# Performance work log

Measured on AMD Instinct MI355X. Metric: run time of the kernel, lower is better.

Reference implementation:

```python
import jax, jax.numpy as jnp
import numpy as np

EMBED_DIM = 512
NUM_HEADS = 8
HEAD_DIM = EMBED_DIM // NUM_HEADS
FFN_DIM = 4 * EMBED_DIM
B, S = 4, 2048
LN_EPS = 1e-5


def _linear_params(key, fan_in, fan_out):
    kw, kb = jax.random.split(key)
    bound = 1.0 / np.sqrt(fan_in)
    W = jax.random.uniform(kw, (fan_in, fan_out), jnp.float32, -bound, bound)
    b = jax.random.uniform(kb, (fan_out,), jnp.float32, -bound, bound)
    return W, b


def setup_inputs() -> dict:
    key = jax.random.key(0)
    ks = jax.random.split(key, 10)
    query = jax.random.normal(ks[0], (B, S, EMBED_DIM), jnp.float32)
    key_t = jax.random.normal(ks[1], (B, S, EMBED_DIM), jnp.float32)
    value = jax.random.normal(ks[2], (B, S, EMBED_DIM), jnp.float32)
    Wq, bq = _linear_params(ks[3], EMBED_DIM, EMBED_DIM)
    Wk, bk = _linear_params(ks[4], EMBED_DIM, EMBED_DIM)
    Wv, bv = _linear_params(ks[5], EMBED_DIM, EMBED_DIM)
    Wo, bo = _linear_params(ks[6], EMBED_DIM, EMBED_DIM)
    W1, b1 = _linear_params(ks[7], EMBED_DIM, FFN_DIM)
    W2, b2 = _linear_params(ks[8], FFN_DIM, EMBED_DIM)
    g1 = jnp.ones((EMBED_DIM,), jnp.float32); be1 = jnp.zeros((EMBED_DIM,), jnp.float32)
    g2 = jnp.ones((EMBED_DIM,), jnp.float32); be2 = jnp.zeros((EMBED_DIM,), jnp.float32)
    return dict(query=query, key=key_t, value=value,
                Wq=Wq, bq=bq, Wk=Wk, bk=bk, Wv=Wv, bv=bv, Wo=Wo, bo=bo,
                g1=g1, be1=be1, g2=g2, be2=be2,
                W1=W1, b1=b1, W2=W2, b2=b2)


def _layernorm(x, g, b):
    mu = jnp.mean(x, axis=-1, keepdims=True)
    var = jnp.mean(jnp.square(x - mu), axis=-1, keepdims=True)
    return (x - mu) * jax.lax.rsqrt(var + LN_EPS) * g + b


def reference(query, key, value, Wq, bq, Wk, bk, Wv, bv, Wo, bo,
              g1, be1, g2, be2, W1, b1, W2, b2):
    b_, s_ = query.shape[:2]
    # projections -> [B, H, S, Dh]
    Q = (query @ Wq + bq).reshape(b_, -1, NUM_HEADS, HEAD_DIM).transpose(0, 2, 1, 3)
    K = (key @ Wk + bk).reshape(b_, -1, NUM_HEADS, HEAD_DIM).transpose(0, 2, 1, 3)
    V = (value @ Wv + bv).reshape(b_, -1, NUM_HEADS, HEAD_DIM).transpose(0, 2, 1, 3)
    scores = jnp.einsum('bhqd,bhkd->bhqk', Q, K) / jnp.sqrt(jnp.float32(HEAD_DIM))
    attn = jax.nn.softmax(scores, axis=-1)  # dropout is eval-mode identity
    ctx = jnp.einsum('bhqk,bhkd->bhqd', attn, V)
    ctx = ctx.transpose(0, 2, 1, 3).reshape(b_, -1, EMBED_DIM)
    out = ctx @ Wo + bo
    out = _layernorm(query + out, g1, be1)
    ffn = jax.nn.gelu(out @ W1 + b1, approximate=False) @ W2 + b2
    return _layernorm(out + ffn, g2, be2)
```

## Files before the change

### kernel.cpp

```cpp
#include <hip/hip_runtime.h>
#include <hip/hip_bf16.h>
#include <math.h>

#define EMBED 512
#define NHEAD 8
#define HDIM 64
#define FFN 2048
#define BB 4
#define SS 2048
#define MROWS (BB*SS)
#define NB ((size_t)MROWS * EMBED)
#define LN_EPS 1e-5f
#define QSCALE 0.180336880111f

typedef __attribute__((ext_vector_type(8))) short short8;
typedef __attribute__((ext_vector_type(4))) float floatx4;

__device__ inline float bf2f(__hip_bfloat16 x) { return __bfloat162float(x); }
__device__ inline __hip_bfloat16 f2bf(float x) { return __float2bfloat16(x); }

__device__ inline float gelu_f(float x) {
    return 0.5f * x * (1.0f + erff(x * 0.70710678118654752f));
}

__device__ inline void async_copy16(const void* g, void* l) {
    __builtin_amdgcn_global_load_lds(
        (const __attribute__((address_space(1))) void*)g,
        (__attribute__((address_space(3))) void*)l, 16, 0, 0);
}

__device__ inline int sane_f(float v) {
    return (v == v) && (fabsf(v) > 0x1p-40f) && (fabsf(v) < 0x1p40f);
}

__global__ void detect_kernel(const void* __restrict__ q, int* __restrict__ flag) {
    const float* qf = (const float*)q;
    int lane = threadIdx.x;
    float v = qf[lane * 1024 + 7];
    bool ok = sane_f(v);
    unsigned long long m = __ballot(ok);
    if (lane == 0) *flag = (__popcll(m) >= 32) ? 1 : 0;
}

__global__ __launch_bounds__(256) void prep_kernel(
    const void* __restrict__ query, const void* __restrict__ keyi, const void* __restrict__ vali,
    const void* __restrict__ Wq, const void* __restrict__ Wk, const void* __restrict__ Wv,
    const void* __restrict__ Wo, const void* __restrict__ W1, const void* __restrict__ W2,
    const void* __restrict__ bq, const void* __restrict__ bk, const void* __restrict__ bv,
    const void* __restrict__ bo, const void* __restrict__ b1, const void* __restrict__ b2,
    const void* __restrict__ g1, const void* __restrict__ be1,
    const void* __restrict__ g2, const void* __restrict__ be2,
    __hip_bfloat16* __restrict__ qkvbf,
    __hip_bfloat16* __restrict__ Wcat,
    __hip_bfloat16* __restrict__ biasb)
{
    __shared__ __hip_bfloat16 L[64][65];
    const int f32 = sane_f(((const float*)query)[7]) + sane_f(((const float*)query)[1031]) +
                    sane_f(((const float*)query)[200003]) + sane_f(((const float*)query)[1000003]) >= 3;
    const int t = threadIdx.x;
    const int blk = blockIdx.x;

    if (blk < 6144) {
        size_t pos = ((size_t)blk * 256 + t) * 8;
        int sel = (int)(pos >> 22);
        size_t off = pos & (NB - 1);
        const void* src = sel == 0 ? query : sel == 1 ? keyi : vali;
        if (f32) {
            const float* s = (const float*)src + off;
            float4 f0 = *reinterpret_cast<const float4*>(s);
            float4 f1 = *reinterpret_cast<const float4*>(s + 4);
            alignas(16) __hip_bfloat16 h[8] = {
                f2bf(f0.x), f2bf(f0.y), f2bf(f0.z), f2bf(f0.w),
                f2bf(f1.x), f2bf(f1.y), f2bf(f1.z), f2bf(f1.w)};
            *reinterpret_cast<uint4*>(qkvbf + pos) = *reinterpret_cast<const uint4*>(h);
        } else {
            *reinterpret_cast<uint4*>(qkvbf + pos) =
                *reinterpret_cast<const uint4*>((const __hip_bfloat16*)src + off);
        }
        return;
    }

    const void* src; __hip_bfloat16* dst; int R, C, r0, c0;
    if (blk < 6400) {
        int b2i = blk - 6144; src = W1; dst = Wcat + 4 * 512 * 512;
        R = 512; C = 2048; r0 = (b2i >> 5) * 64; c0 = (b2i & 31) * 64;
    } else if (blk < 6656) {
        int b3 = blk - 6400; src = W2; dst = Wcat + 4 * 512 * 512 + 512 * 2048;
        R = 2048; C = 512; r0 = (b3 >> 3) * 64; c0 = (b3 & 7) * 64;
    } else if (blk < 6912) {
        int b4 = blk - 6656; int which = b4 >> 6; int tile = b4 & 63;
        src = which == 0 ? Wq : which == 1 ? Wk : which == 2 ? Wv : Wo;
        dst = Wcat + (size_t)which * 512 * 512;
        R = 512; C = 512; r0 = (tile >> 3) * 64; c0 = (tile & 7) * 64;
    } else {
        const void* srcs[10] = {bq, bk, bv, bo, b1, b2, g1, be1, g2, be2};
        const int offs[10] = {0, 512, 1024, 1536, 2048, 4096, 4608, 5120, 5632, 6144};
        const int lens[10] = {512, 512, 512, 512, 2048, 512, 512, 512, 512, 512};
        for (int a = 0; a < 10; ++a)
            for (int i = t; i < lens[a]; i += 256)
                biasb[offs[a] + i] = f32 ? f2bf(((const float*)srcs[a])[i])
                                         : ((const __hip_bfloat16*)srcs[a])[i];
        return;
    }
    for (int c = t; c < 4096; c += 256) {
        int lr = c >> 6, lc = c & 63;
        L[lr][lc] = f32 ? f2bf(((const float*)src)[(size_t)(r0 + lr) * C + c0 + lc])
                        : ((const __hip_bfloat16*)src)[(size_t)(r0 + lr) * C + c0 + lc];
    }
    __syncthreads();
    for (int c = t; c < 4096; c += 256) {
        int lr = c >> 6, lc = c & 63;
        dst[(size_t)(c0 + lr) * R + r0 + lc] = L[lc][lr];
    }
}

template<int ACT, int BIAS>
__global__ __launch_bounds__(256) void gemm_bt_lds_kernel(
    const __hip_bfloat16* __restrict__ A,
    const __hip_bfloat16* __restrict__ Bt,
    const __hip_bfloat16* __restrict__ bias,
    __hip_bfloat16* __restrict__ C,
    int M, int N, int K, int ksplit)
{
    const int bm = blockIdx.x * 128;
    const int bn = blockIdx.y * 128;
    int kbeg = 0, kend = K;
    if (BIAS == 0) {
        kbeg = blockIdx.z * ksplit;
        kend = kbeg + ksplit;
        C += (size_t)blockIdx.z * NB;
    }
    const int t = threadIdx.x;
    const int wave = t >> 6, lane = t & 63;
    const int wm = (wave >> 1) * 64, wn = (wave & 1) * 64;
    const int quad = lane >> 4, r = lane & 15;

    __shared__ alignas(16) __hip_bfloat16 As[2][128 * 32];
    __shared__ alignas(16) __hip_bfloat16 Bs[2][128 * 32];

    floatx4 acc[4][4];
    #pragma unroll
    for (int i = 0; i < 4; ++i)
        #pragma unroll
        for (int j = 0; j < 4; ++j)
            acc[i][j] = (floatx4){0.f, 0.f, 0.f, 0.f};

    const int c0 = wave * 128;

    for (int kt = kbeg; kt < kend; kt += 64) {
        #pragma unroll
        for (int h = 0; h < 2; ++h) {
            #pragma unroll
            for (int it = 0; it < 2; ++it) {
                int c = c0 + it * 64 + lane;
                int row = c >> 2, col = (c & 3) * 8;
                async_copy16(A + (size_t)(bm + row) * K + kt + h * 32 + col,
                             As[h] + (size_t)(c0 + it * 64) * 8);
                async_copy16(Bt + (size_t)(bn + row) * K + kt + h * 32 + col,
                             Bs[h] + (size_t)(c0 + it * 64) * 8);
            }
        }
        __syncthreads();
        #pragma unroll
        for (int h = 0; h < 2; ++h) {
            short8 af[4], bfr[4];
            #pragma unroll
            for (int i = 0; i < 4; ++i)
                af[i] = *reinterpret_cast<const short8*>(&As[h][(wm + i * 16 + r) * 32 + quad * 8]);
            #pragma unroll
            for (int j = 0; j < 4; ++j)
                bfr[j] = *reinterpret_cast<const short8*>(&Bs[h][(wn + j * 16 + r) * 32 + quad * 8]);
            #pragma unroll
            for (int i = 0; i < 4; ++i)
                #pragma unroll
                for (int j = 0; j < 4; ++j)
                    acc[i][j] = __builtin_amdgcn_mfma_f32_16x16x32_bf16(af[i], bfr[j], acc[i][j], 0, 0, 0);
        }
        __syncthreads();
    }

    #pragma unroll
    for (int j = 0; j < 4; ++j) {
        const int n = bn + wn + j * 16 + r;
        float bvv = BIAS ? bf2f(bias[n]) : 0.f;
        #pragma unroll
        for (int i = 0; i < 4; ++i) {
            #pragma unroll
            for (int v = 0; v < 4; ++v) {
                int m = bm + wm + i * 16 + quad * 4 + v;
                float x = acc[i][j][v] + bvv;
                if (ACT == 1) x = gelu_f(x);
                C[(size_t)m * N + n] = f2bf(x);
            }
        }
    }
}

__global__ __launch_bounds__(256) void gemm_qkv_fused_kernel(
    const __hip_bfloat16* __restrict__ Acat,
    const __hip_bfloat16* __restrict__ Wcat,
    const __hip_bfloat16* __restrict__ biascat,
    __hip_bfloat16* __restrict__ Ocat)
{
    const int sel = blockIdx.x >> 6;
    const __hip_bfloat16* A = Acat + (size_t)sel * NB;
    const __hip_bfloat16* Bt = Wcat + (size_t)sel * 512 * 512;
    const __hip_bfloat16* bias = biascat + sel * 512;
    __hip_bfloat16* C = Ocat + (size_t)sel * NB;

    const int bm = (blockIdx.x & 63) * 128;
    const int bn = blockIdx.y * 128;
    const int t = threadIdx.x;
    const int wave = t >> 6, lane = t & 63;
    const int wm = (wave >> 1) * 64, wn = (wave & 1) * 64;
    const int quad = lane >> 4, r = lane & 15;
    const int K = EMBED, N = EMBED;

    __shared__ alignas(16) __hip_bfloat16 As[2][128 * 32];
    __shared__ alignas(16) __hip_bfloat16 Bs[2][128 * 32];

    floatx4 acc[4][4];
    #pragma unroll
    for (int i = 0; i < 4; ++i)
        #pragma unroll
        for (int j = 0; j < 4; ++j)
            acc[i][j] = (floatx4){0.f, 0.f, 0.f, 0.f};

    const int c0 = wave * 128;

    for (int kt = 0; kt < K; kt += 64) {
        #pragma unroll
        for (int h = 0; h < 2; ++h) {
            #pragma unroll
            for (int it = 0; it < 2; ++it) {
                int c = c0 + it * 64 + lane;
                int row = c >> 2, col = (c & 3) * 8;
                async_copy16(A + (size_t)(bm + row) * K + kt + h * 32 + col,
                             As[h] + (size_t)(c0 + it * 64) * 8);
                async_copy16(Bt + (size_t)(bn + row) * K + kt + h * 32 + col,
                             Bs[h] + (size_t)(c0 + it * 64) * 8);
            }
        }
        __syncthreads();
        #pragma unroll
        for (int h = 0; h < 2; ++h) {
            short8 af[4], bfr[4];
            #pragma unroll
            for (int i = 0; i < 4; ++i)
                af[i] = *reinterpret_cast<const short8*>(&As[h][(wm + i * 16 + r) * 32 + quad * 8]);
            #pragma unroll
            for (int j = 0; j < 4; ++j)
                bfr[j] = *reinterpret_cast<const short8*>(&Bs[h][(wn + j * 16 + r) * 32 + quad * 8]);
            #pragma unroll
            for (int i = 0; i < 4; ++i)
                #pragma unroll
                for (int j = 0; j < 4; ++j)
                    acc[i][j] = __builtin_amdgcn_mfma_f32_16x16x32_bf16(af[i], bfr[j], acc[i][j], 0, 0, 0);
        }
        __syncthreads();
    }

    #pragma unroll
    for (int j = 0; j < 4; ++j) {
        const int n = bn + wn + j * 16 + r;
        const float bvv = bf2f(bias[n]);
        #pragma unroll
        for (int i = 0; i < 4; ++i) {
            #pragma unroll
            for (int v = 0; v < 4; ++v) {
                int m = bm + wm + i * 16 + quad * 4 + v;
                C[(size_t)m * N + n] = f2bf(acc[i][j][v] + bvv);
            }
        }
    }
}

__global__ __launch_bounds__(256) void vtrans_kernel(
    const __hip_bfloat16* __restrict__ Vb, __hip_bfloat16* __restrict__ Vt)
{
    const int bh = blockIdx.y;
    const int b = bh >> 3, h = bh & 7;
    const int s0 = blockIdx.x * 64;
    __shared__ alignas(16) __hip_bfloat16 L[64][72];
    const int t = threadIdx.x;
    for (int c = t; c < 512; c += 256) {
        int row = c >> 3, g = c & 7;
        *reinterpret_cast<uint4*>(&L[row][g * 8]) =
            *reinterpret_cast<const uint4*>(Vb + (size_t)(b * SS + s0 + row) * EMBED + h * 64 + g * 8);
    }
    __syncthreads();
    for (int c = t; c < 512; c += 256) {
        int d = c >> 3, g = c & 7;
        alignas(16) __hip_bfloat16 tmp[8];
        #pragma unroll
        for (int j = 0; j < 8; ++j) tmp[j] = L[g * 8 + j][d];
        *reinterpret_cast<uint4*>(Vt + ((size_t)bh * 64 + d) * SS + s0 + g * 8) =
            *reinterpret_cast<const uint4*>(tmp);
    }
}

__global__ __launch_bounds__(256) void attn_mfma_kernel(
    const __hip_bfloat16* __restrict__ Qg,
    const __hip_bfloat16* __restrict__ Kg,
    const __hip_bfloat16* __restrict__ Vt,
    __hip_bfloat16* __restrict__ Apart0,
    __hip_bfloat16* __restrict__ Apart1,
    float* __restrict__ lbuf)
{
    const int bh = blockIdx.y;
    const int b = bh >> 3, h = bh & 7;
    const int q0 = blockIdx.x * 128;
    const int z = blockIdx.z;
    const int t = threadIdx.x;
    const int w = t >> 6, lane = t & 63;
    const int quad = lane >> 4, r = lane & 15;

    __shared__ alignas(16) __hip_bfloat16 Ks[2][64 * 32];
    __shared__ alignas(16) __hip_bfloat16 Vs[2][64 * 32];
    __shared__ alignas(16) __hip_bfloat16 Ps[4][32][72];

    const size_t bbase = (size_t)b * SS * EMBED;
    const size_t hoff = (size_t)h * HDIM;
    const size_t vtbase = (size_t)bh * HDIM * SS;

    short8 aq[2][2];
    #pragma unroll
    for (int s = 0; s < 2; ++s) {
        const __hip_bfloat16* qrow = Qg + bbase + (size_t)(q0 + w * 32 + s * 16 + r) * EMBED + hoff;
        short8 t0 = *reinterpret_cast<const short8*>(qrow + quad * 8);
        short8 t1 = *reinterpret_cast<const short8*>(qrow + 32 + quad * 8);
        #pragma unroll
        for (int i = 0; i < 8; ++i) {
            ((__hip_bfloat16*)&aq[s][0])[i] = f2bf(bf2f(((const __hip_bfloat16*)&t0)[i]) * QSCALE);
            ((__hip_bfloat16*)&aq[s][1])[i] = f2bf(bf2f(((const __hip_bfloat16*)&t1)[i]) * QSCALE);
        }
    }

    const short one = 0x3F80;
    const short8 bones = {one, one, one, one, one, one, one, one};

    const int tensor = w >> 1, slab = w & 1;
    const int srow = lane >> 2, scol = (lane & 3) * 8;

    floatx4 o0[4], o1[4], l0a, l1a;
    #pragma unroll
    for (int nt = 0; nt < 4; ++nt) {
        o0[nt] = (floatx4){0.f, 0.f, 0.f, 0.f};
        o1[nt] = (floatx4){0.f, 0.f, 0.f, 0.f};
    }
    l0a = (floatx4){0.f, 0.f, 0.f, 0.f};
    l1a = (floatx4){0.f, 0.f, 0.f, 0.f};

    const int kbeg = z * (SS / 2), kend = kbeg + SS / 2;
    const __hip_bfloat16* kp[4];
    const __hip_bfloat16* vp[4];
    #pragma unroll
    for (int g = 0; g < 4; ++g) {
        int row = g * 16 + srow;
        kp[g] = Kg + bbase + (size_t)(kbeg + row) * EMBED + hoff + slab * 32 + scol;
        vp[g] = Vt + vtbase + (size_t)row * SS + kbeg + slab * 32 + scol;
    }

    for (int kt = kbeg; kt < kend; kt += 64) {
        __syncthreads();
        if (tensor == 0) {
            #pragma unroll
            for (int g = 0; g < 4; ++g) {
                async_copy16(kp[g], &Ks[slab][g * 512]);
                kp[g] += 64 * EMBED;
            }
        } else {
            #pragma unroll
            for (int g = 0; g < 4; ++g) {
                async_copy16(vp[g], &Vs[slab][g * 512]);
                vp[g] += 64;
            }
        }
        __syncthreads();

        floatx4 s0[4], s1[4];
        #pragma unroll
        for (int nt = 0; nt < 4; ++nt) {
            s0[nt] = (floatx4){0.f, 0.f, 0.f, 0.f};
            s1[nt] = (floatx4){0.f, 0.f, 0.f, 0.f};
        }
        #pragma unroll
        for (int nt = 0; nt < 4; ++nt) {
            short8 ak0 = *reinterpret_cast<const short8*>(&Ks[0][(nt * 16 + r) * 32 + quad * 8]);
            short8 ak1 = *reinterpret_cast<const short8*>(&Ks[1][(nt * 16 + r) * 32 + quad * 8]);
            s0[nt] = __builtin_amdgcn_mfma_f32_16x16x32_bf16(ak0, aq[0][0], s0[nt], 0, 0, 0);
            s0[nt] = __builtin_amdgcn_mfma_f32_16x16x32_bf16(ak1, aq[0][1], s0[nt], 0, 0, 0);
            s1[nt] = __builtin_amdgcn_mfma_f32_16x16x32_bf16(ak0, aq[1][0], s1[nt], 0, 0, 0);
            s1[nt] = __builtin_amdgcn_mfma_f32_16x16x32_bf16(ak1, aq[1][1], s1[nt], 0, 0, 0);
        }

        #pragma unroll
        for (int s = 0; s < 2; ++s) {
            floatx4* sc = s == 0 ? s0 : s1;
            #pragma unroll
            for (int nt = 0; nt < 4; ++nt) {
                float p0 = exp2f(sc[nt][0]), p1 = exp2f(sc[nt][1]);
                float p2 = exp2f(sc[nt][2]), p3 = exp2f(sc[nt][3]);
                __hip_bfloat162 pa = __float22bfloat162_rn(make_float2(p0, p1));
                __hip_bfloat162 pb = __float22bfloat162_rn(make_float2(p2, p3));
                uint2 u;
                u.x = *reinterpret_cast<unsigned*>(&pa);
                u.y = *reinterpret_cast<unsigned*>(&pb);
                *reinterpret_cast<uint2*>(&Ps[w][s * 16 + r][nt * 16 + quad * 4]) = u;
            }
        }

        short8 ap00 = *reinterpret_cast<const short8*>(&Ps[w][r][quad * 8]);
        short8 ap01 = *reinterpret_cast<const short8*>(&Ps[w][r][32 + quad * 8]);
        short8 ap10 = *reinterpret_cast<const short8*>(&Ps[w][16 + r][quad * 8]);
        short8 ap11 = *reinterpret_cast<const short8*>(&Ps[w][16 + r][32 + quad * 8]);
        #pragma unroll
        for (int nt = 0; nt < 4; ++nt) {
            short8 bv0 = *reinterpret_cast<const short8*>(&Vs[0][(nt * 16 + r) * 32 + quad * 8]);
            short8 bv1 = *reinterpret_cast<const short8*>(&Vs[1][(nt * 16 + r) * 32 + quad * 8]);
            o0[nt] = __builtin_amdgcn_mfma_f32_16x16x32_bf16(ap00, bv0, o0[nt], 0, 0, 0);
            o0[nt] = __builtin_amdgcn_mfma_f32_16x16x32_bf16(ap01, bv1, o0[nt], 0, 0, 0);
            o1[nt] = __builtin_amdgcn_mfma_f32_16x16x32_bf16(ap10, bv0, o1[nt], 0, 0, 0);
            o1[nt] = __builtin_amdgcn_mfma_f32_16x16x32_bf16(ap11, bv1, o1[nt], 0, 0, 0);
        }
        l0a = __builtin_amdgcn_mfma_f32_16x16x32_bf16(ap00, bones, l0a, 0, 0, 0);
        l0a = __builtin_amdgcn_mfma_f32_16x16x32_bf16(ap01, bones, l0a, 0, 0, 0);
        l1a = __builtin_amdgcn_mfma_f32_16x16x32_bf16(ap10, bones, l1a, 0, 0, 0);
        l1a = __builtin_amdgcn_mfma_f32_16x16x32_bf16(ap11, bones, l1a, 0, 0, 0);
    }

    __hip_bfloat16* Ap = z == 0 ? Apart0 : Apart1;
    #pragma unroll
    for (int s = 0; s < 2; ++s) {
        floatx4* oa = s == 0 ? o0 : o1;
        floatx4 la = s == 0 ? l0a : l1a;
        #pragma unroll
        for (int v = 0; v < 4; ++v) {
            int q = q0 + w * 32 + s * 16 + quad * 4 + v;
            __hip_bfloat16* orow = Ap + bbase + (size_t)q * EMBED + hoff;
            #pragma unroll
            for (int nt = 0; nt < 4; ++nt)
                orow[nt * 16 + r] = f2bf(oa[nt][v]);
            if (r == 0)
                lbuf[((size_t)z * 32 + bh) * SS + q] = la[v];
        }
    }
}

__global__ __launch_bounds__(256) void attn_combine_kernel(
    const __hip_bfloat16* __restrict__ Apart0,
    const __hip_bfloat16* __restrict__ Apart1,
    const float* __restrict__ lbuf,
    __hip_bfloat16* __restrict__ ctx)
{
    const int bh = blockIdx.y;
    const int b = bh >> 3, h = bh & 7;
    const int q0 = blockIdx.x * 64;
    const int t = threadIdx.x;
    __shared__ float winv[64];

    if (t < 64) {
        float l0 = lbuf[(size_t)bh * SS + q0 + t];
        float l1 = lbuf[((size_t)32 + bh) * SS + q0 + t];
        winv[t] = 1.0f / (l0 + l1);
    }
    __syncthreads();

    const size_t base = (size_t)b * SS * EMBED + (size_t)h * HDIM;
    for (int c = t; c < 512; c += 256) {
        int q = c >> 3, d8 = (c & 7) * 8;
        size_t off = base + (size_t)(q0 + q) * EMBED + d8;
        short8 a0v = *reinterpret_cast<const short8*>(Apart0 + off);
        short8 a1v = *reinterpret_cast<const short8*>(Apart1 + off);
        float si = winv[q];
        alignas(16) __hip_bfloat16 o[8];
        #pragma unroll
        for (int j = 0; j < 8; ++j) {
            float x0 = bf2f(((const __hip_bfloat16*)&a0v)[j]);
            float x1 = bf2f(((const __hip_bfloat16*)&a1v)[j]);
            o[j] = f2bf((x0 + x1) * si);
        }
        *reinterpret_cast<uint4*>(ctx + off) = *reinterpret_cast<const uint4*>(o);
    }
}

__device__ inline float block_reduce_sum(float v, float* sbuf) {
    #pragma unroll
    for (int off = 32; off; off >>= 1) v += __shfl_xor(v, off, 64);
    int wave = threadIdx.x >> 6;
    if ((threadIdx.x & 63) == 0) sbuf[wave] = v;
    __syncthreads();
    float r = sbuf[0] + sbuf[1] + sbuf[2] + sbuf[3];
    __syncthreads();
    return r;
}

template<int OUT32>
__global__ __launch_bounds__(256) void add_ln_split_kernel(
    const __hip_bfloat16* __restrict__ X,
    const __hip_bfloat16* __restrict__ Y0,
    const __hip_bfloat16* __restrict__ Y1,
    const __hip_bfloat16* __restrict__ bias,
    const __hip_bfloat16* __restrict__ g,
    const __hip_bfloat16* __restrict__ bt,
    void* __restrict__ out,
    const int* __restrict__ dflag)
{
    __shared__ float sbuf[4];
    const int row = blockIdx.x;
    const size_t base = (size_t)row * EMBED;
    const int t = threadIdx.x;

    float x0 = bf2f(X[base + t]) + bf2f(Y0[base + t]) + bf2f(Y1[base + t]) + bf2f(bias[t]);
    float x1 = bf2f(X[base + t + 256]) + bf2f(Y0[base + t + 256]) + bf2f(Y1[base + t + 256]) + bf2f(bias[t + 256]);
    float s = block_reduce_sum(x0 + x1, sbuf);
    float mu = s * (1.0f / EMBED);
    float d0 = x0 - mu, d1 = x1 - mu;
    float vs = block_reduce_sum(d0 * d0 + d1 * d1, sbuf);
    float rstd = rsqrtf(vs * (1.0f / EMBED) + LN_EPS);

    float o0 = d0 * rstd * bf2f(g[t]) + bf2f(bt[t]);
    float o1 = d1 * rstd * bf2f(g[t + 256]) + bf2f(bt[t + 256]);
    if (OUT32 && *dflag) {
        ((float*)out)[base + t] = o0;
        ((float*)out)[base + t + 256] = o1;
    } else {
        ((__hip_bfloat16*)out)[base + t] = f2bf(o0);
        ((__hip_bfloat16*)out)[base + t + 256] = f2bf(o1);
    }
}

extern "C" void kernel_launch(void* const* d_in, const int* in_sizes, int n_in,
                              void* d_out, int out_size, void* d_ws, size_t ws_size,
                              hipStream_t stream)
{
    (void)in_sizes; (void)n_in; (void)out_size; (void)ws_size;

    const void* query = d_in[0];
    const void* keyi  = d_in[1];
    const void* vali  = d_in[2];
    const void* Wq = d_in[3];  const void* bq = d_in[4];
    const void* Wk = d_in[5];  const void* bk = d_in[6];
    const void* Wv = d_in[7];  const void* bv = d_in[8];
    const void* Wo = d_in[9];  const void* bo = d_in[10];
    const void* g1 = d_in[11]; const void* be1 = d_in[12];
    const void* g2 = d_in[13]; const void* be2 = d_in[14];
    const void* W1 = d_in[15]; const void* b1 = d_in[16];
    const void* W2 = d_in[17]; const void* b2 = d_in[18];

    int* dflag = (int*)d_ws;
    __hip_bfloat16* biasb = (__hip_bfloat16*)((char*)d_ws + 64);
    __hip_bfloat16* Wcat = biasb + 8192;
    __hip_bfloat16* buf = Wcat + 4 * 512 * 512 + 2 * 512 * 2048;
    __hip_bfloat16* bqkvb = biasb;
    __hip_bfloat16* bob  = biasb + 1536;
    __hip_bfloat16* b1b  = biasb + 2048;
    __hip_bfloat16* b2b  = biasb + 4096;
    __hip_bfloat16* g1b  = biasb + 4608;
    __hip_bfloat16* be1b = biasb + 5120;
    __hip_bfloat16* g2b  = biasb + 5632;
    __hip_bfloat16* be2b = biasb + 6144;
    __hip_bfloat16* qkvbf  = buf;
    __hip_bfloat16* QKVo   = buf + 3 * NB;
    __hip_bfloat16* Qb = QKVo;
    __hip_bfloat16* Kb = QKVo + NB;
    __hip_bfloat16* Vb = QKVo + 2 * NB;
    __hip_bfloat16* Vt     = buf + 1 * NB;
    __hip_bfloat16* Apart0 = buf + 2 * NB;
    __hip_bfloat16* Apart1 = buf + 6 * NB;
    float*          lbuf   = (float*)(buf + 7 * NB);
    __hip_bfloat16* ctx    = buf + 3 * NB;
    __hip_bfloat16* Yw     = buf + 4 * NB;
    __hip_bfloat16* x1     = buf + 3 * NB;
    __hip_bfloat16* hbf    = buf + 4 * NB;
    __hip_bfloat16* Yf     = buf + 1 * NB;

    detect_kernel<<<1, 64, 0, stream>>>(query, dflag);

    prep_kernel<<<6913, 256, 0, stream>>>(
        query, keyi, vali, Wq, Wk, Wv, Wo, W1, W2,
        bq, bk, bv, bo, b1, b2, g1, be1, g2, be2,
        qkvbf, Wcat, biasb);

    gemm_qkv_fused_kernel<<<dim3(192, 4), 256, 0, stream>>>(qkvbf, Wcat, bqkvb, QKVo);

    vtrans_kernel<<<dim3(SS / 64, BB * NHEAD), 256, 0, stream>>>(Vb, Vt);

    attn_mfma_kernel<<<dim3(SS / 128, BB * NHEAD, 2), 256, 0, stream>>>(
        Qb, Kb, Vt, Apart0, Apart1, lbuf);
    attn_combine_kernel<<<dim3(SS / 64, BB * NHEAD), 256, 0, stream>>>(
        Apart0, Apart1, lbuf, ctx);

    gemm_bt_lds_kernel<0, 0><<<dim3(MROWS / 128, EMBED / 128, 2), 256, 0, stream>>>(
        ctx, Wcat + 3 * 512 * 512, nullptr, Yw, MROWS, EMBED, EMBED, EMBED / 2);
    add_ln_split_kernel<0><<<MROWS, 256, 0, stream>>>(
        qkvbf, Yw, Yw + NB, bob, g1b, be1b, x1, dflag);

    gemm_bt_lds_kernel<1, 1><<<dim3(MROWS / 128, FFN / 128), 256, 0, stream>>>(
        x1, Wcat + 4 * 512 * 512, b1b, hbf, MROWS, FFN, EMBED, 0);
    gemm_bt_lds_kernel<0, 0><<<dim3(MROWS / 128, EMBED / 128, 2), 256, 0, stream>>>(
        hbf, Wcat + 4 * 512 * 512 + 512 * 2048, nullptr, Yf, MROWS, EMBED, FFN, FFN / 2);
    add_ln_split_kernel<1><<<MROWS, 256, 0, stream>>>(
        x1, Yf, Yf + NB, b2b, g2b, be2b, d_out, dflag);
}
```

Measured before the change: 343.4 us.

## Swizzle attention K/V LDS layout and make layernorm one wave per row

The K and V tiles in LDS are stored with an XOR swizzle on the 16-byte column chunk, and the MFMA operand reads apply the same swizzle, so a wave's reads spread across LDS banks instead of conflicting. The add+layernorm kernel now gives each 64-lane wave one row with 8 elements per lane. It loads with 16-byte vector accesses and reduces with wave shuffles only, so the shared-memory block reductions and barriers go away. Risk: the swizzle must match the async copy store path exactly, or K and V will be read in the wrong order.

After: 331.7 us. -3.4%, faster.

```diff
diff --git a/kernel.cpp b/kernel.cpp
--- a/kernel.cpp
+++ b/kernel.cpp
@@ -340,7 +340,9 @@
     const short8 bones = {one, one, one, one, one, one, one, one};
 
     const int tensor = w >> 1, slab = w & 1;
-    const int srow = lane >> 2, scol = (lane & 3) * 8;
+    const int srow = lane >> 2;
+    const int scol = (((lane & 3) ^ ((srow >> 1) & 3)) * 8);
+    const int cs = ((r >> 1) & 3) * 8;
 
     floatx4 o0[4], o1[4], l0a, l1a;
     #pragma unroll
@@ -386,8 +388,8 @@
         }
         #pragma unroll
         for (int nt = 0; nt < 4; ++nt) {
-            short8 ak0 = *reinterpret_cast<const short8*>(&Ks[0][(nt * 16 + r) * 32 + quad * 8]);
-            short8 ak1 = *reinterpret_cast<const short8*>(&Ks[1][(nt * 16 + r) * 32 + quad * 8]);
+            short8 ak0 = *reinterpret_cast<const short8*>(&Ks[0][(nt * 16 + r) * 32 + (quad * 8 ^ cs)]);
+            short8 ak1 = *reinterpret_cast<const short8*>(&Ks[1][(nt * 16 + r) * 32 + (quad * 8 ^ cs)]);
             s0[nt] = __builtin_amdgcn_mfma_f32_16x16x32_bf16(ak0, aq[0][0], s0[nt], 0, 0, 0);
             s0[nt] = __builtin_amdgcn_mfma_f32_16x16x32_bf16(ak1, aq[0][1], s0[nt], 0, 0, 0);
             s1[nt] = __builtin_amdgcn_mfma_f32_16x16x32_bf16(ak0, aq[1][0], s1[nt], 0, 0, 0);
@@ -416,8 +418,8 @@
         short8 ap11 = *reinterpret_cast<const short8*>(&Ps[w][16 + r][32 + quad * 8]);
         #pragma unroll
         for (int nt = 0; nt < 4; ++nt) {
-            short8 bv0 = *reinterpret_cast<const short8*>(&Vs[0][(nt * 16 + r) * 32 + quad * 8]);
-            short8 bv1 = *reinterpret_cast<const short8*>(&Vs[1][(nt * 16 + r) * 32 + quad * 8]);
+            short8 bv0 = *reinterpret_cast<const short8*>(&Vs[0][(nt * 16 + r) * 32 + (quad * 8 ^ cs)]);
+            short8 bv1 = *reinterpret_cast<const short8*>(&Vs[1][(nt * 16 + r) * 32 + (quad * 8 ^ cs)]);
             o0[nt] = __builtin_amdgcn_mfma_f32_16x16x32_bf16(ap00, bv0, o0[nt], 0, 0, 0);
             o0[nt] = __builtin_amdgcn_mfma_f32_16x16x32_bf16(ap01, bv1, o0[nt], 0, 0, 0);
             o1[nt] = __builtin_amdgcn_mfma_f32_16x16x32_bf16(ap10, bv0, o1[nt], 0, 0, 0);
@@ -482,17 +484,6 @@
         }
         *reinterpret_cast<uint4*>(ctx + off) = *reinterpret_cast<const uint4*>(o);
     }
-}
-
-__device__ inline float block_reduce_sum(float v, float* sbuf) {
-    #pragma unroll
-    for (int off = 32; off; off >>= 1) v += __shfl_xor(v, off, 64);
-    int wave = threadIdx.x >> 6;
-    if ((threadIdx.x & 63) == 0) sbuf[wave] = v;
-    __syncthreads();
-    float r = sbuf[0] + sbuf[1] + sbuf[2] + sbuf[3];
-    __syncthreads();
-    return r;
 }
 
 template<int OUT32>
@@ -506,27 +497,52 @@
     void* __restrict__ out,
     const int* __restrict__ dflag)
 {
-    __shared__ float sbuf[4];
-    const int row = blockIdx.x;
-    const size_t base = (size_t)row * EMBED;
-    const int t = threadIdx.x;
-
-    float x0 = bf2f(X[base + t]) + bf2f(Y0[base + t]) + bf2f(Y1[base + t]) + bf2f(bias[t]);
-    float x1 = bf2f(X[base + t + 256]) + bf2f(Y0[base + t + 256]) + bf2f(Y1[base + t + 256]) + bf2f(bias[t + 256]);
-    float s = block_reduce_sum(x0 + x1, sbuf);
-    float mu = s * (1.0f / EMBED);
-    float d0 = x0 - mu, d1 = x1 - mu;
-    float vs = block_reduce_sum(d0 * d0 + d1 * d1, sbuf);
-    float rstd = rsqrtf(vs * (1.0f / EMBED) + LN_EPS);
-
-    float o0 = d0 * rstd * bf2f(g[t]) + bf2f(bt[t]);
-    float o1 = d1 * rstd * bf2f(g[t + 256]) + bf2f(bt[t + 256]);
+    const int w = threadIdx.x >> 6, lane = threadIdx.x & 63;
+    const int row = blockIdx.x * 4 + w;
+    const size_t base = (size_t)row * EMBED + lane * 8;
+    const int co = lane * 8;
+
+    short8 xv  = *reinterpret_cast<const short8*>(X + base);
+    short8 y0v = *reinterpret_cast<const short8*>(Y0 + base);
+    short8 y1v = *reinterpret_cast<const short8*>(Y1 + base);
+    short8 bv  = *reinterpret_cast<const short8*>(bias + co);
+
+    float x[8];
+    float s = 0.f;
+    #pragma unroll
+    for (int j = 0; j < 8; ++j) {
+        x[j] = bf2f(((const __hip_bfloat16*)&xv)[j]) + bf2f(((const __hip_bfloat16*)&y0v)[j])
+             + bf2f(((const __hip_bfloat16*)&y1v)[j]) + bf2f(((const __hip_bfloat16*)&bv)[j]);
+        s += x[j];
+    }
+    #pragma unroll
+    for (int off = 32; off; off >>= 1) s += __shfl_xor(s, off, 64);
+    const float mu = s * (1.0f / EMBED);
+    float vs = 0.f;
+    #pragma unroll
+    for (int j = 0; j < 8; ++j) { x[j] -= mu; vs += x[j] * x[j]; }
+    #pragma unroll
+    for (int off = 32; off; off >>= 1) vs += __shfl_xor(vs, off, 64);
+    const float rstd = rsqrtf(vs * (1.0f / EMBED) + LN_EPS);
+
+    short8 gv  = *reinterpret_cast<const short8*>(g + co);
+    short8 btv = *reinterpret_cast<const short8*>(bt + co);
     if (OUT32 && *dflag) {
-        ((float*)out)[base + t] = o0;
-        ((float*)out)[base + t + 256] = o1;
+        float4 o0, o1;
+        float of[8];
+        #pragma unroll
+        for (int j = 0; j < 8; ++j)
+            of[j] = x[j] * rstd * bf2f(((const __hip_bfloat16*)&gv)[j]) + bf2f(((const __hip_bfloat16*)&btv)[j]);
+        o0 = make_float4(of[0], of[1], of[2], of[3]);
+        o1 = make_float4(of[4], of[5], of[6], of[7]);
+        *reinterpret_cast<float4*>((float*)out + base) = o0;
+        *reinterpret_cast<float4*>((float*)out + base + 4) = o1;
     } else {
-        ((__hip_bfloat16*)out)[base + t] = f2bf(o0);
-        ((__hip_bfloat16*)out)[base + t + 256] = f2bf(o1);
+        alignas(16) __hip_bfloat16 o[8];
+        #pragma unroll
+        for (int j = 0; j < 8; ++j)
+            o[j] = f2bf(x[j] * rstd * bf2f(((const __hip_bfloat16*)&gv)[j]) + bf2f(((const __hip_bfloat16*)&btv)[j]));
+        *reinterpret_cast<uint4*>((__hip_bfloat16*)out + base) = *reinterpret_cast<const uint4*>(o);
     }
 }
 
@@ -593,13 +609,13 @@
 
     gemm_bt_lds_kernel<0, 0><<<dim3(MROWS / 128, EMBED / 128, 2), 256, 0, stream>>>(
         ctx, Wcat + 3 * 512 * 512, nullptr, Yw, MROWS, EMBED, EMBED, EMBED / 2);
-    add_ln_split_kernel<0><<<MROWS, 256, 0, stream>>>(
+    add_ln_split_kernel<0><<<MROWS / 4, 256, 0, stream>>>(
         qkvbf, Yw, Yw + NB, bob, g1b, be1b, x1, dflag);
 
     gemm_bt_lds_kernel<1, 1><<<dim3(MROWS / 128, FFN / 128), 256, 0, stream>>>(
         x1, Wcat + 4 * 512 * 512, b1b, hbf, MROWS, FFN, EMBED, 0);
     gemm_bt_lds_kernel<0, 0><<<dim3(MROWS / 128, EMBED / 128, 2), 256, 0, stream>>>(
         hbf, Wcat + 4 * 512 * 512 + 512 * 2048, nullptr, Yf, MROWS, EMBED, FFN, FFN / 2);
-    add_ln_split_kernel<1><<<MROWS, 256, 0, stream>>>(
+    add_ln_split_kernel<1><<<MROWS / 4, 256, 0, stream>>>(
         x1, Yf, Yf + NB, b2b, g2b, be2b, d_out, dflag);
 }
```
